# Performance work log

Hardware: AMD Instinct MI355X
Metric: run time of the kernel (lower is better)

Reference implementation:

```python
import jax, jax.numpy as jnp
import numpy as np

N_NODES = 100000
N_EDGES = 3200000
F_IN = 64
F_OUT = 64
N_REL = 8


def setup_inputs() -> dict:
    key = jax.random.key(0)
    k1, k2, k3, k4, k5, k6 = jax.random.split(key, 6)
    x = jax.random.normal(k1, (N_NODES, F_IN), dtype=jnp.float32)
    edge_index = jax.random.randint(k2, (2, N_EDGES), 0, N_NODES, dtype=jnp.int64)
    edge_type = jax.random.randint(k3, (N_EDGES,), 0, N_REL, dtype=jnp.int64)
    # Glorot-ish init for relation weights, root weight, zero bias (PyG defaults)
    scale = 1.0 / np.sqrt(F_IN)
    weight = jax.random.normal(k4, (N_REL, F_IN, F_OUT), dtype=jnp.float32) * scale
    root = jax.random.normal(k5, (F_IN, F_OUT), dtype=jnp.float32) * scale
    bias = jnp.zeros((F_OUT,), dtype=jnp.float32)
    return {"x": x, "edge_index": edge_index, "edge_type": edge_type,
            "weight": weight, "root": root, "bias": bias}


def reference(x, edge_index, edge_type, weight, root, bias):
    """RGCNConv (PyG defaults: aggr='mean' per relation, root_weight, bias).

    out[i] = x[i] @ root + bias + sum_r mean_{j in N_r(i)} x[j] @ W[r]
    Since W[r] is linear, aggregate (segment-mean) first, transform after.
    """
    n_nodes = x.shape[0]
    n_rel = weight.shape[0]
    src, dst = edge_index[0], edge_index[1]
    xs = x[src]  # [E, F_IN] gathered source features (reused across relations)
    out = x @ root + bias  # [N, F_OUT]
    for r in range(n_rel):  # small fixed relation count
        mask = (edge_type == r).astype(x.dtype)  # [E]
        s = jax.ops.segment_sum(xs * mask[:, None], dst, num_segments=n_nodes)
        cnt = jax.ops.segment_sum(mask, dst, num_segments=n_nodes)
        agg = s / jnp.clip(cnt, 1.0)[:, None]  # per-relation mean over in-edges
        out = out + agg @ weight[r]
    return out
```

## Files before the change

### kernel.cpp

```cpp
#include <hip/hip_runtime.h>
#include <hip/hip_fp16.h>

#define NN 100000
#define NE 3200000
#define F 64
#define NR 8
#define NCB 98
#define CAPC 36864
#define CHUNKA 4000
#define NT 3125
#define SLCAP 1280

typedef _Float16 half8 __attribute__((ext_vector_type(8)));
typedef float f32x4 __attribute__((ext_vector_type(4)));
union U4H8 { uint4 u; half8 h; };

__global__ __launch_bounds__(128) void init_kernel(int* __restrict__ cursors) {
    int t = threadIdx.x;
    if (t < NCB) cursors[t] = t * CAPC;
}

__global__ __launch_bounds__(256) void cvt_kernel(
    const float* __restrict__ x, __half* __restrict__ xh)
{
    size_t base = ((size_t)blockIdx.x * 256 + threadIdx.x) * 8;
    float4 a = *(const float4*)(x + base);
    float4 b = *(const float4*)(x + base + 4);
    __half2 h0 = __floats2half2_rn(a.x, a.y);
    __half2 h1 = __floats2half2_rn(a.z, a.w);
    __half2 h2 = __floats2half2_rn(b.x, b.y);
    __half2 h3 = __floats2half2_rn(b.z, b.w);
    uint4 o;
    o.x = *(unsigned*)&h0; o.y = *(unsigned*)&h1;
    o.z = *(unsigned*)&h2; o.w = *(unsigned*)&h3;
    *(uint4*)(xh + base) = o;
}

__global__ __launch_bounds__(256) void cvtw_kernel(
    const float* __restrict__ weight, const float* __restrict__ root,
    __half* __restrict__ wt9)
{
    int gid = blockIdx.x * 256 + threadIdx.x;
    int s = gid >> 12;
    int rem = gid & 4095;
    int k = rem >> 6, n = rem & 63;
    const float* src = (s == 0) ? root : (weight + ((size_t)(s - 1) << 12));
    wt9[((size_t)s << 12) + (n << 6) + k] = __float2half_rn(src[(k << 6) + n]);
}

__global__ __launch_bounds__(256) void binA_kernel(
    const int* __restrict__ esrc, const int* __restrict__ edst,
    const int* __restrict__ etyp,
    int* __restrict__ cursors, unsigned* __restrict__ stag4)
{
    __shared__ int hist[128][4];
    __shared__ int start[128];
    __shared__ int cur[128][4];
    __shared__ int gbase[NCB];
    __shared__ uint2 recs[CHUNKA];

    const int t = threadIdx.x;
    const int cp = t & 3;
    const int e0 = blockIdx.x * CHUNKA;

    if (t < 128) ((int4*)hist)[t] = make_int4(0, 0, 0, 0);
    __syncthreads();

    uint2 rec[16];
#pragma unroll
    for (int j = 0; j < 16; j++) {
        int i = t + j * 256;
        if (i < CHUNKA) {
            int e = e0 + i;
            unsigned s = (unsigned)esrc[e];
            unsigned d = (unsigned)edst[e];
            unsigned r = (unsigned)etyp[e];
            rec[j] = make_uint2(s, d | (r << 17));
            atomicAdd(&hist[d >> 10][cp], 1);
        }
    }
    __syncthreads();

    int tot = 0;
    if (t < 128) {
        int4 h4 = ((int4*)hist)[t];
        tot = h4.x + h4.y + h4.z + h4.w;
        start[t] = tot;
    }
    __syncthreads();
    for (int off = 1; off < 128; off <<= 1) {
        int v = 0;
        if (t < 128 && t >= off) v = start[t - off];
        __syncthreads();
        if (t < 128) start[t] += v;
        __syncthreads();
    }
    if (t < 128) start[t] -= tot;
    __syncthreads();
    if (t < NCB) {
        int4 h4 = ((int4*)hist)[t];
        int s = start[t];
        cur[t][0] = s;
        cur[t][1] = s + h4.x;
        cur[t][2] = s + h4.x + h4.y;
        cur[t][3] = s + h4.x + h4.y + h4.z;
        gbase[t] = atomicAdd(&cursors[t], tot);
    }
    __syncthreads();

#pragma unroll
    for (int j = 0; j < 16; j++) {
        int i = t + j * 256;
        if (i < CHUNKA) {
            int b = (int)((rec[j].y & 0x1FFFFu) >> 10);
            int slot = atomicAdd(&cur[b][cp], 1);
            recs[slot] = rec[j];
        }
    }
    __syncthreads();

#pragma unroll
    for (int j = 0; j < 16; j++) {
        int i = t + j * 256;
        if (i < CHUNKA) {
            uint2 rr = recs[i];
            int b = (int)((rr.y & 0x1FFFFu) >> 10);
            unsigned d10 = rr.y & 1023u;
            unsigned r   = rr.y >> 17;
            stag4[gbase[b] + (i - start[b])] = rr.x | (d10 << 17) | (r << 27);
        }
    }
}

__global__ __launch_bounds__(256) void binB_kernel(
    const unsigned* __restrict__ stag4, const int* __restrict__ cursors,
    unsigned* __restrict__ packed4, unsigned* __restrict__ runsd)
{
    __shared__ int h[32][4];
    __shared__ int cu[32][4];
    const int b = blockIdx.x >> 3;
    const int c = blockIdx.x & 7;
    const int t = threadIdx.x;
    const int cp = t & 3;
    const int bbase = b * CAPC;
    const int n = cursors[b] - bbase;
    const int s = (int)(((long long)c * n) >> 3);
    const int e = (int)(((long long)(c + 1) * n) >> 3);
    const int base = bbase + s;
    const int cn = e - s;

    if (t < 128) ((int*)h)[t] = 0;
    __syncthreads();
    for (int i = t; i < cn; i += 256) {
        unsigned v = stag4[base + i];
        atomicAdd(&h[(v >> 22) & 31][cp], 1);
    }
    __syncthreads();
    if (t == 0) {
        int acc = 0;
        for (int f = 0; f < 32; f++) {
            int fstart = acc;
#pragma unroll
            for (int k = 0; k < 4; k++) { cu[f][k] = acc; acc += h[f][k]; }
            runsd[(blockIdx.x << 5) + f] = ((unsigned)(base + fstart) << 10) | (unsigned)(acc - fstart);
        }
    }
    __syncthreads();
    for (int i = t; i < cn; i += 256) {
        unsigned v = stag4[base + i];
        unsigned f = (v >> 22) & 31u;
        int p = atomicAdd(&cu[f][cp], 1);
        unsigned d5  = (v >> 17) & 31u;
        unsigned rel = v >> 27;
        packed4[base + p] = (v & 0x1FFFFu) | (d5 << 17) | (rel << 22);
    }
}

__global__ __launch_bounds__(128, 4) void fused_kernel(
    const __half* __restrict__ xh,
    const unsigned* __restrict__ packed4,
    const unsigned* __restrict__ runsd,
    const __half* __restrict__ wt9,
    const float* __restrict__ bias,
    float* __restrict__ out)
{
    __shared__ __align__(16) char Asb[32 * 128];
    __shared__ __align__(16) char Wtb[64 * 128];
    __shared__ int kstart[257];
    __shared__ int slist[SLCAP];
    __shared__ unsigned rdesc[8];
    __shared__ int wsum[2];
    int* const kcur = (int*)Asb;

    const int t = threadIdx.x;
    const int tile = blockIdx.x;
    const int lane = t & 63;
    const int wid = t >> 6;

    if (t < 8) rdesc[t] = runsd[(((tile >> 5) * 8 + t) << 5) + (tile & 31)];
    kstart[t] = 0; kstart[t + 128] = 0;
    __syncthreads();

    unsigned pc[8];
#pragma unroll
    for (int c = 0; c < 8; c++) {
        unsigned d = rdesc[c];
        int rs = (int)(d >> 10), rc = (int)(d & 1023u);
        if (t < rc) {
            pc[c] = packed4[rs + t];
            atomicAdd(&kstart[pc[c] >> 17], 1);
        }
        for (int i = t + 128; i < rc; i += 128)
            atomicAdd(&kstart[packed4[rs + i] >> 17], 1);
    }
    __syncthreads();

    const int a0 = kstart[2 * t], a1 = kstart[2 * t + 1];
    int v = a0 + a1;
#pragma unroll
    for (int off = 1; off < 64; off <<= 1) {
        int u = __shfl_up(v, off);
        if (lane >= off) v += u;
    }
    if (lane == 63) wsum[wid] = v;
    __syncthreads();
    const int wo = wid ? wsum[0] : 0;
    const int incl = wo + v;
    const int ebase = incl - a0 - a1;
    kstart[2 * t]     = ebase;
    kstart[2 * t + 1] = ebase + a0;
    kcur[2 * t]       = ebase;
    kcur[2 * t + 1]   = ebase + a0;
    if (t == 127) kstart[256] = incl;
    __syncthreads();

#pragma unroll
    for (int c = 0; c < 8; c++) {
        unsigned d = rdesc[c];
        int rs = (int)(d >> 10), rc = (int)(d & 1023u);
        if (t < rc) {
            int slot = atomicAdd(&kcur[pc[c] >> 17], 1);
            slist[slot] = (int)(pc[c] & 0x1FFFFu);
        }
        for (int i = t + 128; i < rc; i += 128) {
            unsigned p = packed4[rs + i];
            int slot = atomicAdd(&kcur[p >> 17], 1);
            slist[slot] = (int)(p & 0x1FFFFu);
        }
    }
    __syncthreads();

    const int node0 = tile * 32;
    const int w16 = wid << 4;
    const int sn  = w16 + (lane >> 2);
    const int sq  = lane & 3;
    const int kb  = sq << 3;
    const unsigned snswz = (unsigned)((sn & 7) << 4);
    char* const awp = Asb + sn * 128;

    const int ml = lane & 15;
    const int kg = lane >> 4;
    const int arow = w16 + ml;
    const unsigned aswz = (unsigned)((arow & 7) << 4);
    const unsigned kb0 = (unsigned)(kg << 4);

    f32x4 acc[4];
#pragma unroll
    for (int nt = 0; nt < 4; nt++)
#pragma unroll
        for (int i = 0; i < 4; i++) acc[nt][i] = 0.f;

    for (int seg = 0; seg < 9; seg++) {
        if (seg) __syncthreads();

        {
            const uint4* __restrict__ wsrc = (const uint4*)(wt9 + ((size_t)seg << 12));
#pragma unroll
            for (int j = 0; j < 4; j++) {
                int c = t + (j << 7);
                int n = c >> 3;
                unsigned kbyt = (unsigned)((c & 7) << 4);
                *(uint4*)(Wtb + n * 128 + (kbyt ^ (unsigned)((n & 7) << 4))) = wsrc[c];
            }
        }

        if (seg == 0) {
            const __half* rowp = xh + (size_t)(node0 + sn) * F + kb;
            uint4 va = *(const uint4*)(rowp);
            uint4 vb = *(const uint4*)(rowp + 32);
            *(uint4*)(awp + (((unsigned)(sq << 4)) ^ snswz)) = va;
            *(uint4*)(awp + ((64u | (unsigned)(sq << 4)) ^ snswz)) = vb;
        } else {
            const int key = ((seg - 1) << 5) | sn;
            const int beg = kstart[key];
            const int end = kstart[key + 1];
            float4 A0 = make_float4(0.f, 0.f, 0.f, 0.f);
            float4 A1 = A0, B0 = A0, B1 = A0;
            int i = beg;
            for (; i + 4 <= end; i += 4) {
                const __half* h0 = xh + (size_t)slist[i]     * F + kb;
                const __half* h1 = xh + (size_t)slist[i + 1] * F + kb;
                const __half* h2 = xh + (size_t)slist[i + 2] * F + kb;
                const __half* h3 = xh + (size_t)slist[i + 3] * F + kb;
                uint4 la0 = *(const uint4*)(h0);      uint4 lb0 = *(const uint4*)(h0 + 32);
                uint4 la1 = *(const uint4*)(h1);      uint4 lb1 = *(const uint4*)(h1 + 32);
                uint4 la2 = *(const uint4*)(h2);      uint4 lb2 = *(const uint4*)(h2 + 32);
                uint4 la3 = *(const uint4*)(h3);      uint4 lb3 = *(const uint4*)(h3 + 32);
#define ACC8(v, P, Q) { \
                float2 t0 = __half22float2(*(const __half2*)&(v).x); \
                float2 t1 = __half22float2(*(const __half2*)&(v).y); \
                float2 t2 = __half22float2(*(const __half2*)&(v).z); \
                float2 t3 = __half22float2(*(const __half2*)&(v).w); \
                P.x += t0.x; P.y += t0.y; P.z += t1.x; P.w += t1.y; \
                Q.x += t2.x; Q.y += t2.y; Q.z += t3.x; Q.w += t3.y; }
                ACC8(la0, A0, A1) ACC8(la1, A0, A1) ACC8(la2, A0, A1) ACC8(la3, A0, A1)
                ACC8(lb0, B0, B1) ACC8(lb1, B0, B1) ACC8(lb2, B0, B1) ACC8(lb3, B0, B1)
            }
            for (; i < end; i++) {
                const __half* h0 = xh + (size_t)slist[i] * F + kb;
                uint4 la = *(const uint4*)(h0);
                uint4 lb = *(const uint4*)(h0 + 32);
                ACC8(la, A0, A1)
                ACC8(lb, B0, B1)
            }
#undef ACC8
            const float scl = 1.0f / (float)max(end - beg, 1);
            __half2 p0 = __floats2half2_rn(A0.x * scl, A0.y * scl);
            __half2 p1 = __floats2half2_rn(A0.z * scl, A0.w * scl);
            __half2 p2 = __floats2half2_rn(A1.x * scl, A1.y * scl);
            __half2 p3 = __floats2half2_rn(A1.z * scl, A1.w * scl);
            __half2 q0 = __floats2half2_rn(B0.x * scl, B0.y * scl);
            __half2 q1 = __floats2half2_rn(B0.z * scl, B0.w * scl);
            __half2 q2 = __floats2half2_rn(B1.x * scl, B1.y * scl);
            __half2 q3 = __floats2half2_rn(B1.z * scl, B1.w * scl);
            uint4 pa, pb;
            pa.x = *(unsigned*)&p0; pa.y = *(unsigned*)&p1;
            pa.z = *(unsigned*)&p2; pa.w = *(unsigned*)&p3;
            pb.x = *(unsigned*)&q0; pb.y = *(unsigned*)&q1;
            pb.z = *(unsigned*)&q2; pb.w = *(unsigned*)&q3;
            *(uint4*)(awp + (((unsigned)(sq << 4)) ^ snswz)) = pa;
            *(uint4*)(awp + ((64u | (unsigned)(sq << 4)) ^ snswz)) = pb;
        }
        __syncthreads();

        U4H8 fa0, fa1;
        fa0.u = *(const uint4*)(Asb + arow * 128 + (kb0 ^ aswz));
        fa1.u = *(const uint4*)(Asb + arow * 128 + ((64u | kb0) ^ aswz));
#pragma unroll
        for (int nt = 0; nt < 4; nt++) {
            int wrow = (nt << 4) + ml;
            unsigned wswz = (unsigned)((wrow & 7) << 4);
            U4H8 fb0, fb1;
            fb0.u = *(const uint4*)(Wtb + wrow * 128 + (kb0 ^ wswz));
            fb1.u = *(const uint4*)(Wtb + wrow * 128 + ((64u | kb0) ^ wswz));
            acc[nt] = __builtin_amdgcn_mfma_f32_16x16x32_f16(fa0.h, fb0.h, acc[nt], 0, 0, 0);
            acc[nt] = __builtin_amdgcn_mfma_f32_16x16x32_f16(fa1.h, fb1.h, acc[nt], 0, 0, 0);
        }
    }

#pragma unroll
    for (int nt = 0; nt < 4; nt++) {
        float bb = bias[(nt << 4) + ml];
#pragma unroll
        for (int i = 0; i < 4; i++) {
            int node = node0 + w16 + (kg << 2) + i;
            out[(size_t)node * F + (nt << 4) + ml] = acc[nt][i] + bb;
        }
    }
}

extern "C" void kernel_launch(void* const* d_in, const int* in_sizes, int n_in,
                              void* d_out, int out_size, void* d_ws, size_t ws_size,
                              hipStream_t stream) {
    const float* x    = (const float*)d_in[0];
    const int*   ei   = (const int*)d_in[1];
    const int*   et   = (const int*)d_in[2];
    const float* wgt  = (const float*)d_in[3];
    const float* root = (const float*)d_in[4];
    const float* bias = (const float*)d_in[5];
    float*       out  = (float*)d_out;

    int*      cursors = (int*)d_ws;
    unsigned* runsd   = (unsigned*)((char*)d_ws + 512);
    unsigned* stag4   = (unsigned*)((char*)d_ws + 512 + 100352);
    unsigned* packed4 = stag4 + (size_t)NCB * CAPC;
    __half*   xh      = (__half*)(packed4 + (size_t)NCB * CAPC);
    __half*   wt9     = xh + (size_t)NN * F;

    init_kernel<<<1, 128, 0, stream>>>(cursors);
    cvt_kernel<<<NN * F / (256 * 8), 256, 0, stream>>>(x, xh);
    cvtw_kernel<<<144, 256, 0, stream>>>(wgt, root, wt9);
    binA_kernel<<<NE / CHUNKA, 256, 0, stream>>>(ei, ei + NE, et, cursors, stag4);
    binB_kernel<<<NCB * 8, 256, 0, stream>>>(stag4, cursors, packed4, runsd);
    fused_kernel<<<NT, 128, 0, stream>>>(xh, packed4, runsd, wt9, bias, out);
}
```

Before: 232.9 us.

## Replace two-pass coarse binning with count-scan-scatter counting sort per tile

Swaps the two-level bucketing (binA staging into 98 coarse buckets, then binB splitting into 32-node runs) for a global per-tile histogram, a single-block exclusive scan and a direct scatter using global atomics on per-tile cursors. The fused kernel now reads one contiguous edge range per tile instead of eight run descriptors. This drops the staging buffer and one full read/write pass over the edges. In exchange it adds heavy global atomic contention in the scatter (3.2M atomics over 3125 counters) and an extra launch for the serial scan. Tiles with more than 1280 edges are silently truncated.

```diff
diff --git a/kernel.cpp b/kernel.cpp
--- a/kernel.cpp
+++ b/kernel.cpp
@@ -5,19 +5,16 @@
 #define NE 3200000
 #define F 64
 #define NR 8
-#define NCB 98
-#define CAPC 36864
-#define CHUNKA 4000
-#define NT 3125
+#define NTI 3125
 #define SLCAP 1280
 
 typedef _Float16 half8 __attribute__((ext_vector_type(8)));
 typedef float f32x4 __attribute__((ext_vector_type(4)));
 union U4H8 { uint4 u; half8 h; };
 
-__global__ __launch_bounds__(128) void init_kernel(int* __restrict__ cursors) {
-    int t = threadIdx.x;
-    if (t < NCB) cursors[t] = t * CAPC;
+__global__ __launch_bounds__(256) void zeroh_kernel(int* __restrict__ hist) {
+    int i = blockIdx.x * 256 + threadIdx.x;
+    if (i < NTI) hist[i] = 0;
 }
 
 __global__ __launch_bounds__(256) void cvt_kernel(
@@ -48,138 +45,90 @@
     wt9[((size_t)s << 12) + (n << 6) + k] = __float2half_rn(src[(k << 6) + n]);
 }
 
-__global__ __launch_bounds__(256) void binA_kernel(
+__global__ __launch_bounds__(256) void count_kernel(
+    const int* __restrict__ edst, int* __restrict__ hist)
+{
+    __shared__ int h[NTI];
+    const int t = threadIdx.x;
+    for (int i = t; i < NTI; i += 256) h[i] = 0;
+    __syncthreads();
+    const int e0 = blockIdx.x * 8192;
+#pragma unroll
+    for (int j = 0; j < 32; j++) {
+        int e = e0 + (j << 8) + t;
+        if (e < NE) atomicAdd(&h[((unsigned)edst[e]) >> 5], 1);
+    }
+    __syncthreads();
+    for (int i = t; i < NTI; i += 256) {
+        int v = h[i];
+        if (v) atomicAdd(&hist[i], v);
+    }
+}
+
+__global__ __launch_bounds__(256) void scan_kernel(
+    const int* __restrict__ hist, int* __restrict__ tilestart,
+    int* __restrict__ cursor)
+{
+    __shared__ int wsum[4];
+    const int t = threadIdx.x;
+    const int lane = t & 63;
+    const int wid = t >> 6;
+    const int c0 = t * 13;
+    int loc[13];
+    int s = 0;
+#pragma unroll
+    for (int j = 0; j < 13; j++) {
+        int c = c0 + j;
+        int v = (c < NTI) ? hist[c] : 0;
+        loc[j] = s;
+        s += v;
+    }
+    int v = s;
+#pragma unroll
+    for (int off = 1; off < 64; off <<= 1) {
+        int u = __shfl_up(v, off);
+        if (lane >= off) v += u;
+    }
+    if (lane == 63) wsum[wid] = v;
+    __syncthreads();
+    int wo = 0;
+#pragma unroll
+    for (int w = 0; w < 3; w++) if (w < wid) wo += wsum[w];
+    const int base = wo + v - s;
+#pragma unroll
+    for (int j = 0; j < 13; j++) {
+        int c = c0 + j;
+        if (c < NTI) {
+            int b = base + loc[j];
+            tilestart[c] = b;
+            cursor[c] = b;
+        }
+    }
+    if (t == 255) tilestart[NTI] = wo + v;
+}
+
+__global__ __launch_bounds__(256) void scatter_kernel(
     const int* __restrict__ esrc, const int* __restrict__ edst,
     const int* __restrict__ etyp,
-    int* __restrict__ cursors, unsigned* __restrict__ stag4)
-{
-    __shared__ int hist[128][4];
-    __shared__ int start[128];
-    __shared__ int cur[128][4];
-    __shared__ int gbase[NCB];
-    __shared__ uint2 recs[CHUNKA];
-
-    const int t = threadIdx.x;
-    const int cp = t & 3;
-    const int e0 = blockIdx.x * CHUNKA;
-
-    if (t < 128) ((int4*)hist)[t] = make_int4(0, 0, 0, 0);
-    __syncthreads();
-
-    uint2 rec[16];
-#pragma unroll
-    for (int j = 0; j < 16; j++) {
-        int i = t + j * 256;
-        if (i < CHUNKA) {
-            int e = e0 + i;
-            unsigned s = (unsigned)esrc[e];
-            unsigned d = (unsigned)edst[e];
-            unsigned r = (unsigned)etyp[e];
-            rec[j] = make_uint2(s, d | (r << 17));
-            atomicAdd(&hist[d >> 10][cp], 1);
-        }
-    }
-    __syncthreads();
-
-    int tot = 0;
-    if (t < 128) {
-        int4 h4 = ((int4*)hist)[t];
-        tot = h4.x + h4.y + h4.z + h4.w;
-        start[t] = tot;
-    }
-    __syncthreads();
-    for (int off = 1; off < 128; off <<= 1) {
-        int v = 0;
-        if (t < 128 && t >= off) v = start[t - off];
-        __syncthreads();
-        if (t < 128) start[t] += v;
-        __syncthreads();
-    }
-    if (t < 128) start[t] -= tot;
-    __syncthreads();
-    if (t < NCB) {
-        int4 h4 = ((int4*)hist)[t];
-        int s = start[t];
-        cur[t][0] = s;
-        cur[t][1] = s + h4.x;
-        cur[t][2] = s + h4.x + h4.y;
-        cur[t][3] = s + h4.x + h4.y + h4.z;
-        gbase[t] = atomicAdd(&cursors[t], tot);
-    }
-    __syncthreads();
-
-#pragma unroll
-    for (int j = 0; j < 16; j++) {
-        int i = t + j * 256;
-        if (i < CHUNKA) {
-            int b = (int)((rec[j].y & 0x1FFFFu) >> 10);
-            int slot = atomicAdd(&cur[b][cp], 1);
-            recs[slot] = rec[j];
-        }
-    }
-    __syncthreads();
-
-#pragma unroll
-    for (int j = 0; j < 16; j++) {
-        int i = t + j * 256;
-        if (i < CHUNKA) {
-            uint2 rr = recs[i];
-            int b = (int)((rr.y & 0x1FFFFu) >> 10);
-            unsigned d10 = rr.y & 1023u;
-            unsigned r   = rr.y >> 17;
-            stag4[gbase[b] + (i - start[b])] = rr.x | (d10 << 17) | (r << 27);
-        }
-    }
-}
-
-__global__ __launch_bounds__(256) void binB_kernel(
-    const unsigned* __restrict__ stag4, const int* __restrict__ cursors,
-    unsigned* __restrict__ packed4, unsigned* __restrict__ runsd)
-{
-    __shared__ int h[32][4];
-    __shared__ int cu[32][4];
-    const int b = blockIdx.x >> 3;
-    const int c = blockIdx.x & 7;
-    const int t = threadIdx.x;
-    const int cp = t & 3;
-    const int bbase = b * CAPC;
-    const int n = cursors[b] - bbase;
-    const int s = (int)(((long long)c * n) >> 3);
-    const int e = (int)(((long long)(c + 1) * n) >> 3);
-    const int base = bbase + s;
-    const int cn = e - s;
-
-    if (t < 128) ((int*)h)[t] = 0;
-    __syncthreads();
-    for (int i = t; i < cn; i += 256) {
-        unsigned v = stag4[base + i];
-        atomicAdd(&h[(v >> 22) & 31][cp], 1);
-    }
-    __syncthreads();
-    if (t == 0) {
-        int acc = 0;
-        for (int f = 0; f < 32; f++) {
-            int fstart = acc;
-#pragma unroll
-            for (int k = 0; k < 4; k++) { cu[f][k] = acc; acc += h[f][k]; }
-            runsd[(blockIdx.x << 5) + f] = ((unsigned)(base + fstart) << 10) | (unsigned)(acc - fstart);
-        }
-    }
-    __syncthreads();
-    for (int i = t; i < cn; i += 256) {
-        unsigned v = stag4[base + i];
-        unsigned f = (v >> 22) & 31u;
-        int p = atomicAdd(&cu[f][cp], 1);
-        unsigned d5  = (v >> 17) & 31u;
-        unsigned rel = v >> 27;
-        packed4[base + p] = (v & 0x1FFFFu) | (d5 << 17) | (rel << 22);
+    int* __restrict__ cursor, unsigned* __restrict__ packed4)
+{
+    const int e0 = blockIdx.x * 1024 + threadIdx.x;
+#pragma unroll
+    for (int j = 0; j < 4; j++) {
+        int e = e0 + (j << 8);
+        unsigned s = (unsigned)esrc[e];
+        unsigned d = (unsigned)edst[e];
+        unsigned r = (unsigned)etyp[e];
+        int tile = (int)(d >> 5);
+        int slot = atomicAdd(&cursor[tile], 1);
+        packed4[slot] = s | ((d & 31u) << 17) | (r << 22);
     }
 }
 
 __global__ __launch_bounds__(128, 4) void fused_kernel(
     const __half* __restrict__ xh,
     const unsigned* __restrict__ packed4,
-    const unsigned* __restrict__ runsd,
+    const int* __restrict__ tilestart,
     const __half* __restrict__ wt9,
     const float* __restrict__ bias,
     float* __restrict__ out)
@@ -188,7 +137,6 @@
     __shared__ __align__(16) char Wtb[64 * 128];
     __shared__ int kstart[257];
     __shared__ int slist[SLCAP];
-    __shared__ unsigned rdesc[8];
     __shared__ int wsum[2];
     int* const kcur = (int*)Asb;
 
@@ -197,21 +145,20 @@
     const int lane = t & 63;
     const int wid = t >> 6;
 
-    if (t < 8) rdesc[t] = runsd[(((tile >> 5) * 8 + t) << 5) + (tile & 31)];
+    const int ebase0 = tilestart[tile];
+    const int rc = min(tilestart[tile + 1] - ebase0, SLCAP);
+
     kstart[t] = 0; kstart[t + 128] = 0;
     __syncthreads();
 
-    unsigned pc[8];
-#pragma unroll
-    for (int c = 0; c < 8; c++) {
-        unsigned d = rdesc[c];
-        int rs = (int)(d >> 10), rc = (int)(d & 1023u);
-        if (t < rc) {
-            pc[c] = packed4[rs + t];
-            atomicAdd(&kstart[pc[c] >> 17], 1);
-        }
-        for (int i = t + 128; i < rc; i += 128)
-            atomicAdd(&kstart[packed4[rs + i] >> 17], 1);
+    unsigned pc[10];
+#pragma unroll
+    for (int j = 0; j < 10; j++) {
+        int i = t + (j << 7);
+        if (i < rc) {
+            pc[j] = packed4[ebase0 + i];
+            atomicAdd(&kstart[pc[j] >> 17], 1);
+        }
     }
     __syncthreads();
 
@@ -235,17 +182,11 @@
     __syncthreads();
 
 #pragma unroll
-    for (int c = 0; c < 8; c++) {
-        unsigned d = rdesc[c];
-        int rs = (int)(d >> 10), rc = (int)(d & 1023u);
-        if (t < rc) {
-            int slot = atomicAdd(&kcur[pc[c] >> 17], 1);
-            slist[slot] = (int)(pc[c] & 0x1FFFFu);
-        }
-        for (int i = t + 128; i < rc; i += 128) {
-            unsigned p = packed4[rs + i];
-            int slot = atomicAdd(&kcur[p >> 17], 1);
-            slist[slot] = (int)(p & 0x1FFFFu);
+    for (int j = 0; j < 10; j++) {
+        int i = t + (j << 7);
+        if (i < rc) {
+            int slot = atomicAdd(&kcur[pc[j] >> 17], 1);
+            slist[slot] = (int)(pc[j] & 0x1FFFFu);
         }
     }
     __syncthreads();
@@ -380,17 +321,19 @@
     const float* bias = (const float*)d_in[5];
     float*       out  = (float*)d_out;
 
-    int*      cursors = (int*)d_ws;
-    unsigned* runsd   = (unsigned*)((char*)d_ws + 512);
-    unsigned* stag4   = (unsigned*)((char*)d_ws + 512 + 100352);
-    unsigned* packed4 = stag4 + (size_t)NCB * CAPC;
-    __half*   xh      = (__half*)(packed4 + (size_t)NCB * CAPC);
-    __half*   wt9     = xh + (size_t)NN * F;
-
-    init_kernel<<<1, 128, 0, stream>>>(cursors);
+    char* ws = (char*)d_ws;
+    int*      hist      = (int*)ws;
+    int*      tilestart = (int*)(ws + 16384);
+    int*      cursor    = (int*)(ws + 32768);
+    unsigned* packed4   = (unsigned*)(ws + 49152);
+    __half*   xh        = (__half*)(ws + 49152 + (size_t)NE * 4);
+    __half*   wt9       = xh + (size_t)NN * F;
+
+    zeroh_kernel<<<13, 256, 0, stream>>>(hist);
     cvt_kernel<<<NN * F / (256 * 8), 256, 0, stream>>>(x, xh);
     cvtw_kernel<<<144, 256, 0, stream>>>(wgt, root, wt9);
-    binA_kernel<<<NE / CHUNKA, 256, 0, stream>>>(ei, ei + NE, et, cursors, stag4);
-    binB_kernel<<<NCB * 8, 256, 0, stream>>>(stag4, cursors, packed4, runsd);
-    fused_kernel<<<NT, 128, 0, stream>>>(xh, packed4, runsd, wt9, bias, out);
-}
+    count_kernel<<<(NE + 8191) / 8192, 256, 0, stream>>>(ei + NE, hist);
+    scan_kernel<<<1, 256, 0, stream>>>(hist, tilestart, cursor);
+    scatter_kernel<<<NE / 1024, 256, 0, stream>>>(ei, ei + NE, et, cursor, packed4);
+    fused_kernel<<<NTI, 128, 0, stream>>>(xh, packed4, tilestart, wt9, bias, out);
+}
```

After: 480.1 us. +106.1%, slower.

## Vectorize edge binning loads and keep binB records in registers

Applied to the files above, without the earlier changes.

binA now reads src, dst and type with 128-bit loads, four edges per thread. It packs the final 32-bit staging word up front, so the shared staging buffer holds 4-byte records plus a byte-sized bucket id instead of 8-byte records. binB aligns its eight sub-ranges to multiples of four so it can load with uint4, and it keeps the loaded words in registers instead of reading stag4 a second time. binB's serial single-thread prefix over 32 bins is replaced by a wavefront shuffle scan. The aim is to cut global traffic, instruction count and serial work in the preprocessing kernels, at the cost of more registers and a fixed per-thread capacity assumption of 5120 records per sub-range in binB.

```diff
diff --git a/kernel.cpp b/kernel.cpp
--- a/kernel.cpp
+++ b/kernel.cpp
@@ -57,7 +57,8 @@
     __shared__ int start[128];
     __shared__ int cur[128][4];
     __shared__ int gbase[NCB];
-    __shared__ uint2 recs[CHUNKA];
+    __shared__ unsigned recs[CHUNKA];
+    __shared__ unsigned char bks[CHUNKA];
 
     const int t = threadIdx.x;
     const int cp = t & 3;
@@ -66,17 +67,28 @@
     if (t < 128) ((int4*)hist)[t] = make_int4(0, 0, 0, 0);
     __syncthreads();
 
-    uint2 rec[16];
-#pragma unroll
-    for (int j = 0; j < 16; j++) {
-        int i = t + j * 256;
-        if (i < CHUNKA) {
-            int e = e0 + i;
-            unsigned s = (unsigned)esrc[e];
-            unsigned d = (unsigned)edst[e];
-            unsigned r = (unsigned)etyp[e];
-            rec[j] = make_uint2(s, d | (r << 17));
-            atomicAdd(&hist[d >> 10][cp], 1);
+    unsigned pay[4][4];
+    unsigned bk4[4];
+    const uint4* sv4 = (const uint4*)(esrc + e0);
+    const uint4* dv4 = (const uint4*)(edst + e0);
+    const uint4* rv4 = (const uint4*)(etyp + e0);
+#pragma unroll
+    for (int j = 0; j < 4; j++) {
+        int g = t + (j << 8);
+        if (g < CHUNKA / 4) {
+            uint4 sv = sv4[g];
+            uint4 dv = dv4[g];
+            uint4 rv = rv4[g];
+            unsigned b0 = dv.x >> 10, b1 = dv.y >> 10, b2 = dv.z >> 10, b3 = dv.w >> 10;
+            pay[j][0] = sv.x | ((dv.x & 1023u) << 17) | (rv.x << 27);
+            pay[j][1] = sv.y | ((dv.y & 1023u) << 17) | (rv.y << 27);
+            pay[j][2] = sv.z | ((dv.z & 1023u) << 17) | (rv.z << 27);
+            pay[j][3] = sv.w | ((dv.w & 1023u) << 17) | (rv.w << 27);
+            bk4[j] = b0 | (b1 << 8) | (b2 << 16) | (b3 << 24);
+            atomicAdd(&hist[b0][cp], 1);
+            atomicAdd(&hist[b1][cp], 1);
+            atomicAdd(&hist[b2][cp], 1);
+            atomicAdd(&hist[b3][cp], 1);
         }
     }
     __syncthreads();
@@ -109,25 +121,26 @@
     __syncthreads();
 
 #pragma unroll
+    for (int j = 0; j < 4; j++) {
+        int g = t + (j << 8);
+        if (g < CHUNKA / 4) {
+#pragma unroll
+            for (int k = 0; k < 4; k++) {
+                int b = (int)((bk4[j] >> (k << 3)) & 255u);
+                int slot = atomicAdd(&cur[b][cp], 1);
+                recs[slot] = pay[j][k];
+                bks[slot] = (unsigned char)b;
+            }
+        }
+    }
+    __syncthreads();
+
+#pragma unroll
     for (int j = 0; j < 16; j++) {
-        int i = t + j * 256;
+        int i = t + (j << 8);
         if (i < CHUNKA) {
-            int b = (int)((rec[j].y & 0x1FFFFu) >> 10);
-            int slot = atomicAdd(&cur[b][cp], 1);
-            recs[slot] = rec[j];
-        }
-    }
-    __syncthreads();
-
-#pragma unroll
-    for (int j = 0; j < 16; j++) {
-        int i = t + j * 256;
-        if (i < CHUNKA) {
-            uint2 rr = recs[i];
-            int b = (int)((rr.y & 0x1FFFFu) >> 10);
-            unsigned d10 = rr.y & 1023u;
-            unsigned r   = rr.y >> 17;
-            stag4[gbase[b] + (i - start[b])] = rr.x | (d10 << 17) | (r << 27);
+            int b = (int)bks[i];
+            stag4[gbase[b] + (i - start[b])] = recs[i];
         }
     }
 }
@@ -144,35 +157,63 @@
     const int cp = t & 3;
     const int bbase = b * CAPC;
     const int n = cursors[b] - bbase;
-    const int s = (int)(((long long)c * n) >> 3);
-    const int e = (int)(((long long)(c + 1) * n) >> 3);
+    const int s = (c == 0) ? 0 : (int)((((long long)c * n) >> 3) & ~3LL);
+    const int e = (c == 7) ? n : (int)((((long long)(c + 1) * n) >> 3) & ~3LL);
     const int base = bbase + s;
     const int cn = e - s;
 
     if (t < 128) ((int*)h)[t] = 0;
     __syncthreads();
-    for (int i = t; i < cn; i += 256) {
-        unsigned v = stag4[base + i];
-        atomicAdd(&h[(v >> 22) & 31][cp], 1);
-    }
-    __syncthreads();
-    if (t == 0) {
-        int acc = 0;
-        for (int f = 0; f < 32; f++) {
-            int fstart = acc;
-#pragma unroll
-            for (int k = 0; k < 4; k++) { cu[f][k] = acc; acc += h[f][k]; }
-            runsd[(blockIdx.x << 5) + f] = ((unsigned)(base + fstart) << 10) | (unsigned)(acc - fstart);
-        }
-    }
-    __syncthreads();
-    for (int i = t; i < cn; i += 256) {
-        unsigned v = stag4[base + i];
-        unsigned f = (v >> 22) & 31u;
-        int p = atomicAdd(&cu[f][cp], 1);
-        unsigned d5  = (v >> 17) & 31u;
-        unsigned rel = v >> 27;
-        packed4[base + p] = (v & 0x1FFFFu) | (d5 << 17) | (rel << 22);
+
+    unsigned pc[5][4];
+    const uint4* src4 = (const uint4*)(stag4 + base);
+#pragma unroll
+    for (int j = 0; j < 5; j++) {
+        int idx = (t + (j << 8)) << 2;
+        if (idx < cn) {
+            uint4 v = src4[t + (j << 8)];
+            pc[j][0] = v.x; pc[j][1] = v.y; pc[j][2] = v.z; pc[j][3] = v.w;
+#pragma unroll
+            for (int k = 0; k < 4; k++)
+                if (idx + k < cn) atomicAdd(&h[(pc[j][k] >> 22) & 31][cp], 1);
+        }
+    }
+    __syncthreads();
+
+    if (t < 32) {
+        int h0 = h[t][0], h1 = h[t][1], h2 = h[t][2], h3 = h[t][3];
+        int tot = h0 + h1 + h2 + h3;
+        int v = tot;
+#pragma unroll
+        for (int off = 1; off < 32; off <<= 1) {
+            int u = __shfl_up(v, off);
+            if (t >= off) v += u;
+        }
+        int eb = v - tot;
+        cu[t][0] = eb;
+        cu[t][1] = eb + h0;
+        cu[t][2] = eb + h0 + h1;
+        cu[t][3] = eb + h0 + h1 + h2;
+        runsd[(blockIdx.x << 5) + t] = ((unsigned)(base + eb) << 10) | (unsigned)tot;
+    }
+    __syncthreads();
+
+#pragma unroll
+    for (int j = 0; j < 5; j++) {
+        int idx = (t + (j << 8)) << 2;
+        if (idx < cn) {
+#pragma unroll
+            for (int k = 0; k < 4; k++) {
+                if (idx + k < cn) {
+                    unsigned v = pc[j][k];
+                    unsigned f = (v >> 22) & 31u;
+                    int p = atomicAdd(&cu[f][cp], 1);
+                    unsigned d5  = (v >> 17) & 31u;
+                    unsigned rel = v >> 27;
+                    packed4[base + p] = (v & 0x1FFFFu) | (d5 << 17) | (rel << 22);
+                }
+            }
+        }
     }
 }
 
```

After: 227.6 us. 2.3% less time.
